# Kernel optimization log

Hardware: AMD Instinct MI355X
Metric: run time of the kernel (lower is better)

## Reference

```python
import jax, jax.numpy as jnp
import numpy as np

EPS = 1e-6

def _layernorm(x, g, b):
    mu = jnp.mean(x, axis=-1, keepdims=True)
    var = jnp.mean(jnp.square(x - mu), axis=-1, keepdims=True)
    return (x - mu) * jax.lax.rsqrt(var + EPS) * g + b

def _mhsa(xq, xk, xv, mask, Wq, bq, Wk, bk, Wv, bv, Wo, bo, num_heads):
    B, Nq, D = xq.shape
    Nk = xk.shape[1]
    dh = D // num_heads
    # project then split heads: [B, N, D] -> [B, H, N, dh]
    def split(x, W, b, N):
        return (x @ W + b).reshape(B, N, num_heads, dh).transpose(0, 2, 1, 3)
    q = split(xq, Wq, bq, Nq)
    k = split(xk, Wk, bk, Nk)
    v = split(xv, Wv, bv, Nk)
    scores = jnp.einsum('bhnd,bhmd->bhnm', q, k) / jnp.sqrt(jnp.float32(dh))
    if mask is not None:
        scores = scores + mask * (-1e9)
    w = jax.nn.softmax(scores, axis=-1)
    out = jnp.einsum('bhnm,bhmd->bhnd', w, v)          # [B,H,Nq,dh]
    out = out.transpose(0, 2, 1, 3).reshape(B, Nq, D)  # concat heads
    return out @ Wo + bo

def setup_inputs() -> dict:
    B, N, D, FF = 2, 2048, 512, 2048
    key = jax.random.key(0)
    ks = jax.random.split(key, 32)
    std = 0.02
    p = {}
    p['inputs'] = jax.random.normal(ks[0], (B, N, D), jnp.float32)
    p['enc_output'] = jax.random.normal(ks[1], (B, N, D), jnp.float32)
    # causal look-ahead mask: 1 where masked (future positions)
    p['look_ahead_mask'] = jnp.triu(jnp.ones((N, N), jnp.float32), k=1)[None, None]
    p['padding_mask'] = jnp.zeros((B, 1, 1, N), jnp.float32)
    i = 2
    for pre in ('q1', 'k1', 'v1', 'o1', 'q2', 'k2', 'v2', 'o2'):
        p[pre + '_w'] = jax.random.normal(ks[i], (D, D), jnp.float32) * std; i += 1
        p[pre + '_b'] = jnp.zeros((D,), jnp.float32)
    p['f1_w'] = jax.random.normal(ks[i], (D, FF), jnp.float32) * std; i += 1
    p['f1_b'] = jnp.zeros((FF,), jnp.float32)
    p['f2_w'] = jax.random.normal(ks[i], (FF, D), jnp.float32) * std; i += 1
    p['f2_b'] = jnp.zeros((D,), jnp.float32)
    for ln in ('ln1', 'ln2', 'ln3'):
        p[ln + '_g'] = jnp.ones((D,), jnp.float32)
        p[ln + '_b'] = jnp.zeros((D,), jnp.float32)
    p['training'] = 0
    return p

def reference(inputs, enc_output, look_ahead_mask, padding_mask,
              q1_w, q1_b, k1_w, k1_b, v1_w, v1_b, o1_w, o1_b,
              q2_w, q2_b, k2_w, k2_b, v2_w, v2_b, o2_w, o2_b,
              f1_w, f1_b, f2_w, f2_b,
              ln1_g, ln1_b, ln2_g, ln2_b, ln3_g, ln3_b,
              training):
    H = 8
    # self-attention (q=k=v=inputs), causal mask; dropout inactive (eval)
    attn1 = _mhsa(inputs, inputs, inputs, look_ahead_mask,
                  q1_w, q1_b, k1_w, k1_b, v1_w, v1_b, o1_w, o1_b, H)
    out1 = _layernorm(inputs + attn1, ln1_g, ln1_b)
    # cross attention: NOTE original arg order -> q=enc, k=enc, v=out1
    attn2 = _mhsa(enc_output, enc_output, out1, padding_mask,
                  q2_w, q2_b, k2_w, k2_b, v2_w, v2_b, o2_w, o2_b, H)
    out2 = _layernorm(out1 + attn2, ln2_g, ln2_b)
    ffn = jax.nn.relu(out2 @ f1_w + f1_b) @ f2_w + f2_b
    return _layernorm(out2 + ffn, ln3_g, ln3_b)
```

## Files before the change

kernel.cpp:

```cpp
#include <hip/hip_runtime.h>

typedef __attribute__((ext_vector_type(8))) _Float16 half8;
typedef __attribute__((ext_vector_type(4))) _Float16 half4;
typedef __attribute__((ext_vector_type(2))) _Float16 half2_t;
typedef __attribute__((ext_vector_type(2))) __fp16 fp16x2;
typedef __attribute__((ext_vector_type(4))) float f32x4;

#define AS1 __attribute__((address_space(1)))
#define AS3 __attribute__((address_space(3)))

constexpr int SEQ = 2048, DM = 512, FFD = 2048, NH = 8, DH = 64;
constexpr int M = 2 * SEQ;
constexpr float QSCALE = 0.125f * 1.4426950408889634f;

__global__ __launch_bounds__(256)
void preproc(const float* __restrict__ q1_w, const float* __restrict__ k1_w,
             const float* __restrict__ v1_w, const float* __restrict__ o1_w,
             const float* __restrict__ q2_w, const float* __restrict__ k2_w,
             const float* __restrict__ v2_w, const float* __restrict__ o2_w,
             const float* __restrict__ f1_w, const float* __restrict__ f2_w,
             _Float16* __restrict__ qk1t, _Float16* __restrict__ v1t,
             _Float16* __restrict__ o1t, _Float16* __restrict__ qk2t,
             _Float16* __restrict__ v2t, _Float16* __restrict__ o2t,
             _Float16* __restrict__ f1t, _Float16* __restrict__ f2t,
             const float* __restrict__ q1_b, const float* __restrict__ k1_b,
             const float* __restrict__ q2_b, const float* __restrict__ k2_b,
             float* __restrict__ qk1b, float* __restrict__ qk2b,
             const float* __restrict__ inp, const float* __restrict__ enc,
             _Float16* __restrict__ xh, _Float16* __restrict__ eh) {
    __shared__ _Float16 tile[64 * 65];
    const int j = blockIdx.x, tid = threadIdx.x;
    if (j < 1024) {
        const float* src; _Float16* dst; int K, N, n0, k0;
        if (j < 512) {
            int w8 = j >> 6, t = j & 63;
            K = 512; N = 512; n0 = (t & 7) * 64; k0 = (t >> 3) * 64;
            switch (w8) {
                case 0: src = q1_w; dst = qk1t; break;
                case 1: src = k1_w; dst = qk1t + 512 * 512; break;
                case 2: src = v1_w; dst = v1t; break;
                case 3: src = o1_w; dst = o1t; break;
                case 4: src = q2_w; dst = qk2t; break;
                case 5: src = k2_w; dst = qk2t + 512 * 512; break;
                case 6: src = v2_w; dst = v2t; break;
                default: src = o2_w; dst = o2t; break;
            }
        } else if (j < 768) {
            int t = j - 512; K = 512; N = 2048;
            n0 = (t % 32) * 64; k0 = (t / 32) * 64; src = f1_w; dst = f1t;
        } else {
            int t = j - 768; K = 2048; N = 512;
            n0 = (t % 8) * 64; k0 = (t / 8) * 64; src = f2_w; dst = f2t;
        }
        int c = tid & 63, r4 = tid >> 6;
        for (int i = 0; i < 16; i++) {
            int r = r4 * 16 + i;
            tile[r * 65 + c] = (_Float16)src[(size_t)(k0 + r) * N + n0 + c];
        }
        __syncthreads();
        for (int i = 0; i < 16; i++) {
            int r = r4 * 16 + i;
            dst[(size_t)(n0 + r) * K + k0 + c] = tile[c * 65 + r];
        }
    } else if (j == 1024) {
        for (int i = tid; i < 512; i += 256) { qk1b[i] = q1_b[i]; qk1b[512 + i] = k1_b[i]; }
    } else if (j == 1025) {
        for (int i = tid; i < 512; i += 256) { qk2b[i] = q2_b[i]; qk2b[512 + i] = k2_b[i]; }
    } else {
        int k = j - 1026;
        const float* s = (k < 1024) ? inp : enc;
        _Float16* d = (k < 1024) ? xh : eh;
        size_t base = (size_t)(k & 1023) * 2048 + tid * 8;
        f32x4 a = *(const f32x4*)(s + base);
        f32x4 b2 = *(const f32x4*)(s + base + 4);
        half8 h;
        h[0] = (_Float16)a[0]; h[1] = (_Float16)a[1];
        h[2] = (_Float16)a[2]; h[3] = (_Float16)a[3];
        h[4] = (_Float16)b2[0]; h[5] = (_Float16)b2[1];
        h[6] = (_Float16)b2[2]; h[7] = (_Float16)b2[3];
        *(half8*)(d + base) = h;
    }
}

template<int BM, int BN, int WM, int WN, bool RELU, int EPI, int SPLIT>
__global__ __launch_bounds__(256)
void gemm_tn(const _Float16* __restrict__ A, const _Float16* __restrict__ Bt,
             const float* __restrict__ bias,
             float* __restrict__ outF, _Float16* __restrict__ outH,
             _Float16* __restrict__ Qh, _Float16* __restrict__ Kh,
             const _Float16* __restrict__ A2, const _Float16* __restrict__ Bt2,
             const float* __restrict__ bias2,
             _Float16* __restrict__ Qh2, _Float16* __restrict__ Kh2,
             int Mtot, int N, int K) {
    constexpr int ROWS = BM + BN;
    __shared__ _Float16 smem[ROWS * 64];
    constexpr int AF = WM / 16, BF = WN / 16;
    constexpr int WROW = BM / WM;
    const int tid = threadIdx.x;
    const int wid = tid >> 6, lid = tid & 63;
    const int wr = (wid % WROW) * WM;
    const int wc = (wid / WROW) * WN;
    const int mi = lid & 15, qd = lid >> 4;
    const int gx = gridDim.x, gy = gridDim.y;
    const int L = blockIdx.y * gx + blockIdx.x;
    const int by = L % gy, bx = L / gy;
    const int m0 = by * BM, n0 = bx * BN;
    const int Kc = K / SPLIT;
    const int kbase = (SPLIT > 1) ? blockIdx.z * Kc : 0;
    const int job = (EPI == 4) ? blockIdx.z : 0;
    const _Float16* Ap = ((EPI == 4 && job) ? A2 : A) + (size_t)m0 * K + kbase;
    const _Float16* Bp = ((EPI == 4 && job) ? Bt2 : Bt) + (size_t)n0 * K + kbase;
    const float* bsel = (EPI == 4 && job) ? bias2 : bias;
    const int lrow = lid >> 3;
    const int gblk = (lid & 7) ^ ((lid >> 3) & 7);
    auto stage = [&](int kt) {
        #pragma unroll
        for (int l = 0; l < BM / 32; l++) {
            int c = l * 4 + wid;
            int row = c * 8 + lrow;
            __builtin_amdgcn_global_load_lds(
                (const AS1 unsigned int*)(Ap + (size_t)row * K + kt * 64 + gblk * 8),
                (AS3 unsigned int*)&smem[c * 512], 16, 0, 0);
        }
        #pragma unroll
        for (int l = 0; l < BN / 32; l++) {
            int c = l * 4 + wid;
            int row = c * 8 + lrow;
            __builtin_amdgcn_global_load_lds(
                (const AS1 unsigned int*)(Bp + (size_t)row * K + kt * 64 + gblk * 8),
                (AS3 unsigned int*)&smem[BM * 64 + c * 512], 16, 0, 0);
        }
    };
    f32x4 acc[AF][BF] = {};
    const int NIT = Kc / 64;
    stage(0);
    __builtin_amdgcn_s_waitcnt(0x0F70);
    __syncthreads();
    for (int t = 0; t < NIT; t++) {
        #pragma unroll
        for (int h = 0; h < 2; h++) {
            const int sA = ((4 * h + qd) ^ (mi & 7)) * 8;
            half8 af[AF], bfr[BF];
            #pragma unroll
            for (int i = 0; i < AF; i++)
                af[i] = *(const half8*)&smem[(wr + i * 16 + mi) * 64 + sA];
            #pragma unroll
            for (int j = 0; j < BF; j++)
                bfr[j] = *(const half8*)&smem[(BM + wc + j * 16 + mi) * 64 + sA];
            #pragma unroll
            for (int i = 0; i < AF; i++)
                #pragma unroll
                for (int j = 0; j < BF; j++)
                    acc[i][j] = __builtin_amdgcn_mfma_f32_16x16x32_f16(af[i], bfr[j], acc[i][j], 0, 0, 0);
        }
        if (t + 1 < NIT) {
            __syncthreads();
            stage(t + 1);
            __builtin_amdgcn_s_waitcnt(0x0F70);
            __syncthreads();
        }
    }
    float* oF = outF;
    if (SPLIT > 1 && outF) oF = outF + (size_t)blockIdx.z * Mtot * N;
    _Float16* oH = outH;
    if (EPI == 5) oH = outH + (size_t)blockIdx.z * Mtot * N;
    const bool doBias = bsel && (SPLIT == 1 || blockIdx.z == 0);
    #pragma unroll
    for (int i = 0; i < AF; i++) {
        #pragma unroll
        for (int j = 0; j < BF; j++) {
            #pragma unroll
            for (int r = 0; r < 4; r++) {
                int row = m0 + wr + i * 16 + qd * 4 + r;
                int col = n0 + wc + j * 16 + mi;
                float v = acc[i][j][r];
                if (EPI == 3) {
                    v += bsel[row];
                    outH[(size_t)row * N + col] = (_Float16)v;
                } else if (EPI == 4) {
                    if (doBias) v += bsel[col];
                    int hh = (col >> 6) & 7, d = col & 63;
                    int bb = row >> 11, n = row & 2047;
                    size_t idx = (((size_t)bb * 8 + hh) * SEQ + n) * 64 + d;
                    if (col < 512) (job ? Qh2 : Qh)[idx] = (_Float16)(v * QSCALE);
                    else           (job ? Kh2 : Kh)[idx] = (_Float16)v;
                } else if (EPI == 5) {
                    if (doBias) v += bsel[col];
                    oH[(size_t)row * N + col] = (_Float16)v;
                } else {
                    if (doBias) v += bsel[col];
                    if (RELU) v = fmaxf(v, 0.f);
                    size_t off = (size_t)row * N + col;
                    if (oF) oF[off] = v;
                    if (outH) outH[off] = (_Float16)v;
                }
            }
        }
    }
}

template<bool CAUSAL>
__global__ __launch_bounds__(256)
void attn_chunk(const _Float16* __restrict__ Qh, const _Float16* __restrict__ Kh,
                const _Float16* __restrict__ VT, int ldv,
                _Float16* __restrict__ Opart, float* __restrict__ Lpart) {
    const int qt = blockIdx.x, bh = blockIdx.y, c = blockIdx.z;
    int t0, stp, n;
    if (CAUSAL) {
        if (c > qt) return;
        t0 = c; stp = 4; n = (qt - c) / 4 + 1;
    } else {
        t0 = c * 8; stp = 1; n = 8;
    }
    __shared__ _Float16 QPs[64 * 64];
    __shared__ _Float16 Ks[2][64 * 64];
    __shared__ _Float16 Vs[2][64 * 64];
    const int tid = threadIdx.x, w = tid >> 6, lane = tid & 63;
    const int mi = lane & 15, qd = lane >> 4;
    const int qbase = qt * 64;
    const int b = bh >> 3, h = bh & 7;
    const _Float16* Qp = Qh + ((size_t)bh * SEQ + qbase) * 64;
    const _Float16* Kp = Kh + (size_t)bh * SEQ * 64;
    const _Float16* Vp = VT + (size_t)(h * 64) * ldv + (size_t)b * SEQ;
    const int r0 = tid >> 3, blk = tid & 7;
    const int sw = (blk ^ (r0 & 7)) * 8;
    const int lrow = lane >> 3;
    const int gblk = (lane & 7) ^ ((lane >> 3) & 7);
    const int f0 = (qd ^ (mi & 7)) * 8;
    const int f1 = ((qd + 4) ^ (mi & 7)) * 8;

    {
        half8 q0 = *(const half8*)(Qp + r0 * 64 + blk * 8);
        half8 q1 = *(const half8*)(Qp + (r0 + 32) * 64 + blk * 8);
        *(half8*)&QPs[r0 * 64 + sw] = q0;
        *(half8*)&QPs[(r0 + 32) * 64 + sw] = q1;
    }
    auto stageKV = [&](int t, int buf) {
        #pragma unroll
        for (int l = 0; l < 2; l++) {
            int cc = l * 4 + w;
            int row = cc * 8 + lrow;
            __builtin_amdgcn_global_load_lds(
                (const AS1 unsigned int*)(Kp + ((size_t)(t * 64 + row)) * 64 + gblk * 8),
                (AS3 unsigned int*)&Ks[buf][cc * 512], 16, 0, 0);
            __builtin_amdgcn_global_load_lds(
                (const AS1 unsigned int*)(Vp + (size_t)row * ldv + t * 64 + gblk * 8),
                (AS3 unsigned int*)&Vs[buf][cc * 512], 16, 0, 0);
        }
    };
    stageKV(t0, 0);
    __builtin_amdgcn_s_waitcnt(0x0F70);
    __syncthreads();
    half8 qb0 = *(half8*)&QPs[(w * 16 + mi) * 64 + f0];
    half8 qb1 = *(half8*)&QPs[(w * 16 + mi) * 64 + f1];
    f32x4 oacc[4] = {};
    float lacc = 0.f;
    for (int i = 0; i < n; i++) {
        const int t = t0 + i * stp;
        if (i + 1 < n) stageKV(t0 + (i + 1) * stp, (i + 1) & 1);
        const _Float16* ksb = Ks[i & 1];
        const _Float16* vsb = Vs[i & 1];
        f32x4 s[4];
        #pragma unroll
        for (int j = 0; j < 4; j++) {
            half8 ka0 = *(const half8*)&ksb[(j * 16 + mi) * 64 + f0];
            half8 ka1 = *(const half8*)&ksb[(j * 16 + mi) * 64 + f1];
            f32x4 a = {};
            a = __builtin_amdgcn_mfma_f32_16x16x32_f16(ka0, qb0, a, 0, 0, 0);
            a = __builtin_amdgcn_mfma_f32_16x16x32_f16(ka1, qb1, a, 0, 0, 0);
            s[j] = a;
        }
        if (CAUSAL && t == qt) {
            int qg = qbase + w * 16 + mi;
            #pragma unroll
            for (int j = 0; j < 4; j++)
                #pragma unroll
                for (int r = 0; r < 4; r++) {
                    int key = t * 64 + j * 16 + qd * 4 + r;
                    if (key > qg) s[j][r] = -1e30f;
                }
        }
        #pragma unroll
        for (int j = 0; j < 4; j++)
            #pragma unroll
            for (int r = 0; r < 4; r++) {
                float pv = __builtin_amdgcn_exp2f(s[j][r]);
                s[j][r] = pv;
                lacc += pv;
            }
        #pragma unroll
        for (int j = 0; j < 4; j++) {
            fp16x2 lo = __builtin_amdgcn_cvt_pkrtz(s[j][0], s[j][1]);
            fp16x2 hi = __builtin_amdgcn_cvt_pkrtz(s[j][2], s[j][3]);
            half2_t lo2 = __builtin_bit_cast(half2_t, lo);
            half2_t hi2 = __builtin_bit_cast(half2_t, hi);
            half4 pq;
            pq[0] = lo2[0]; pq[1] = lo2[1]; pq[2] = hi2[0]; pq[3] = hi2[1];
            int blkp = (2 * j + (qd >> 1)) ^ (mi & 7);
            *(half4*)&QPs[(w * 16 + mi) * 64 + blkp * 8 + (qd & 1) * 4] = pq;
        }
        half8 pa0 = *(half8*)&QPs[(w * 16 + mi) * 64 + f0];
        half8 pa1 = *(half8*)&QPs[(w * 16 + mi) * 64 + f1];
        #pragma unroll
        for (int j = 0; j < 4; j++) {
            half8 vb0 = *(const half8*)&vsb[(j * 16 + mi) * 64 + f0];
            half8 vb1 = *(const half8*)&vsb[(j * 16 + mi) * 64 + f1];
            oacc[j] = __builtin_amdgcn_mfma_f32_16x16x32_f16(pa0, vb0, oacc[j], 0, 0, 0);
            oacc[j] = __builtin_amdgcn_mfma_f32_16x16x32_f16(pa1, vb1, oacc[j], 0, 0, 0);
        }
        __builtin_amdgcn_s_waitcnt(0x0F70);
        __syncthreads();
    }
    const size_t tb = (((size_t)c * 16 + bh) * 32 + qt) * 4096;
    #pragma unroll
    for (int j = 0; j < 4; j++)
        #pragma unroll
        for (int r = 0; r < 4; r++)
            Opart[tb + (size_t)(w * 16 + qd * 4 + r) * 64 + j * 16 + mi] = (_Float16)oacc[j][r];
    lacc += __shfl_xor(lacc, 16, 64);
    lacc += __shfl_xor(lacc, 32, 64);
    if (qd == 0)
        Lpart[(((size_t)c * 16 + bh) * 32 + qt) * 64 + w * 16 + mi] = lacc;
}

template<bool CAUSAL>
__global__ __launch_bounds__(256)
void attn_combine(const _Float16* __restrict__ Opart, const float* __restrict__ Lpart,
                  _Float16* __restrict__ O) {
    const int qt = blockIdx.x, bh = blockIdx.y;
    const int b = bh >> 3, h = bh & 7;
    const int NC = CAUSAL ? min(qt + 1, 4) : 4;
    const int d = threadIdx.x & 63;
    const int rr = threadIdx.x >> 6;
    for (int it = 0; it < 16; it++) {
        int q = it * 4 + rr;
        float lsum = 0.f, acc = 0.f;
        for (int cc = 0; cc < NC; cc++) {
            lsum += Lpart[(((size_t)cc * 16 + bh) * 32 + qt) * 64 + q];
            acc += (float)Opart[(((size_t)cc * 16 + bh) * 32 + qt) * 4096 + (size_t)q * 64 + d];
        }
        int qrow = qt * 64 + q;
        O[((size_t)(b * SEQ + qrow)) * 512 + h * 64 + d] = (_Float16)(acc / lsum);
    }
}

template<typename RT>
__global__ __launch_bounds__(256)
void add_ln(const RT* __restrict__ res, const _Float16* __restrict__ y,
            size_t pstride, int nparts,
            const float* __restrict__ g, const float* __restrict__ bb,
            float* __restrict__ outF, _Float16* __restrict__ outH) {
    int row = blockIdx.x;
    int tid = threadIdx.x;
    size_t base = (size_t)row * 512;
    float x0 = (float)res[base + tid];
    float x1 = (float)res[base + tid + 256];
    for (int s = 0; s < nparts; s++) {
        x0 += (float)y[s * pstride + base + tid];
        x1 += (float)y[s * pstride + base + tid + 256];
    }
    float s = x0 + x1, sq = x0 * x0 + x1 * x1;
    #pragma unroll
    for (int off = 32; off > 0; off >>= 1) {
        s += __shfl_xor(s, off, 64);
        sq += __shfl_xor(sq, off, 64);
    }
    __shared__ float ls[4], lq[4];
    int w = tid >> 6;
    if ((tid & 63) == 0) { ls[w] = s; lq[w] = sq; }
    __syncthreads();
    s = ls[0] + ls[1] + ls[2] + ls[3];
    sq = lq[0] + lq[1] + lq[2] + lq[3];
    float mu = s * (1.f / 512.f);
    float var = sq * (1.f / 512.f) - mu * mu;
    float rs = rsqrtf(var + 1e-6f);
    float o0 = (x0 - mu) * rs * g[tid] + bb[tid];
    float o1 = (x1 - mu) * rs * g[tid + 256] + bb[tid + 256];
    if (outF) { outF[base + tid] = o0; outF[base + tid + 256] = o1; }
    if (outH) { outH[base + tid] = (_Float16)o0; outH[base + tid + 256] = (_Float16)o1; }
}

extern "C" void kernel_launch(void* const* d_in, const int* in_sizes, int n_in,
                              void* d_out, int out_size, void* d_ws, size_t ws_size,
                              hipStream_t stream) {
    (void)in_sizes; (void)n_in; (void)out_size; (void)ws_size;
    const float* inp  = (const float*)d_in[0];
    const float* enc  = (const float*)d_in[1];
    const float* q1_w = (const float*)d_in[4];
    const float* q1_b = (const float*)d_in[5];
    const float* k1_w = (const float*)d_in[6];
    const float* k1_b = (const float*)d_in[7];
    const float* v1_w = (const float*)d_in[8];
    const float* v1_b = (const float*)d_in[9];
    const float* o1_w = (const float*)d_in[10];
    const float* o1_b = (const float*)d_in[11];
    const float* q2_w = (const float*)d_in[12];
    const float* q2_b = (const float*)d_in[13];
    const float* k2_w = (const float*)d_in[14];
    const float* k2_b = (const float*)d_in[15];
    const float* v2_w = (const float*)d_in[16];
    const float* v2_b = (const float*)d_in[17];
    const float* o2_w = (const float*)d_in[18];
    const float* o2_b = (const float*)d_in[19];
    const float* f1_w = (const float*)d_in[20];
    const float* f1_b = (const float*)d_in[21];
    const float* f2_w = (const float*)d_in[22];
    const float* f2_b = (const float*)d_in[23];
    const float* ln1_g = (const float*)d_in[24];
    const float* ln1_b = (const float*)d_in[25];
    const float* ln2_g = (const float*)d_in[26];
    const float* ln2_b = (const float*)d_in[27];
    const float* ln3_g = (const float*)d_in[28];
    const float* ln3_b = (const float*)d_in[29];

    char* p = (char*)d_ws;
    auto alloc = [&](size_t bytes) { char* r = p; p += (bytes + 255) & ~(size_t)255; return (void*)r; };
    _Float16* xh    = (_Float16*)alloc((size_t)M * DM * 2);
    _Float16* eh    = (_Float16*)alloc((size_t)M * DM * 2);
    _Float16* qk1t  = (_Float16*)alloc((size_t)1024 * DM * 2);
    _Float16* v1t   = (_Float16*)alloc((size_t)DM * DM * 2);
    _Float16* o1t   = (_Float16*)alloc((size_t)DM * DM * 2);
    _Float16* qk2t  = (_Float16*)alloc((size_t)1024 * DM * 2);
    _Float16* v2t   = (_Float16*)alloc((size_t)DM * DM * 2);
    _Float16* o2t   = (_Float16*)alloc((size_t)DM * DM * 2);
    _Float16* f1t   = (_Float16*)alloc((size_t)FFD * DM * 2);
    _Float16* f2t   = (_Float16*)alloc((size_t)DM * FFD * 2);
    float* qk1b     = (float*)alloc(1024 * 4);
    float* qk2b     = (float*)alloc(1024 * 4);
    _Float16* Qh1   = (_Float16*)alloc((size_t)M * DM * 2);
    _Float16* Kh1   = (_Float16*)alloc((size_t)M * DM * 2);
    _Float16* Qh2   = (_Float16*)alloc((size_t)M * DM * 2);
    _Float16* Kh2   = (_Float16*)alloc((size_t)M * DM * 2);
    _Float16* V1T   = (_Float16*)alloc((size_t)DM * M * 2);
    _Float16* V2T   = (_Float16*)alloc((size_t)DM * M * 2);
    _Float16* Ah    = (_Float16*)alloc((size_t)M * DM * 2);
    _Float16* Ph    = (_Float16*)alloc((size_t)2 * M * DM * 2);
    float* Lbuf     = (float*)alloc((size_t)4 * 16 * 32 * 64 * 4);
    _Float16* out1h = (_Float16*)alloc((size_t)M * DM * 2);
    _Float16* out2h = (_Float16*)alloc((size_t)M * DM * 2);
    _Float16* hh    = (_Float16*)alloc((size_t)M * FFD * 2);
    _Float16* OpH   = (_Float16*)alloc((size_t)4 * 16 * 32 * 4096 * 2);
    const size_t PS = (size_t)M * DM;

    dim3 t256(256);
    preproc<<<dim3(1026 + 2048), t256, 0, stream>>>(
        q1_w, k1_w, v1_w, o1_w, q2_w, k2_w, v2_w, o2_w, f1_w, f2_w,
        qk1t, v1t, o1t, qk2t, v2t, o2t, f1t, f2t,
        q1_b, k1_b, q2_b, k2_b, qk1b, qk2b, inp, enc, xh, eh);

    gemm_tn<128, 64, 64, 32, false, 4, 1><<<dim3(16, 32, 2), t256, 0, stream>>>(
        xh, qk1t, qk1b, nullptr, nullptr, Qh1, Kh1,
        eh, qk2t, qk2b, Qh2, Kh2, M, 1024, 512);
    gemm_tn<64, 64, 32, 32, false, 3, 1><<<dim3(64, 8), t256, 0, stream>>>(
        v1t, xh, v1_b, nullptr, V1T, nullptr, nullptr,
        nullptr, nullptr, nullptr, nullptr, nullptr, 512, M, 512);

    attn_chunk<true><<<dim3(32, 16, 4), t256, 0, stream>>>(Qh1, Kh1, V1T, M, OpH, Lbuf);
    attn_combine<true><<<dim3(32, 16), t256, 0, stream>>>(OpH, Lbuf, Ah);
    gemm_tn<64, 64, 32, 32, false, 5, 2><<<dim3(8, 64, 2), t256, 0, stream>>>(
        Ah, o1t, o1_b, nullptr, Ph, nullptr, nullptr,
        nullptr, nullptr, nullptr, nullptr, nullptr, M, 512, 512);
    add_ln<float><<<dim3(M), t256, 0, stream>>>(inp, Ph, PS, 2, ln1_g, ln1_b, nullptr, out1h);

    gemm_tn<64, 64, 32, 32, false, 3, 1><<<dim3(64, 8), t256, 0, stream>>>(
        v2t, out1h, v2_b, nullptr, V2T, nullptr, nullptr,
        nullptr, nullptr, nullptr, nullptr, nullptr, 512, M, 512);
    attn_chunk<false><<<dim3(32, 16, 4), t256, 0, stream>>>(Qh2, Kh2, V2T, M, OpH, Lbuf);
    attn_combine<false><<<dim3(32, 16), t256, 0, stream>>>(OpH, Lbuf, Ah);
    gemm_tn<64, 64, 32, 32, false, 5, 2><<<dim3(8, 64, 2), t256, 0, stream>>>(
        Ah, o2t, o2_b, nullptr, Ph, nullptr, nullptr,
        nullptr, nullptr, nullptr, nullptr, nullptr, M, 512, 512);
    add_ln<_Float16><<<dim3(M), t256, 0, stream>>>(out1h, Ph, PS, 2, ln2_g, ln2_b, nullptr, out2h);

    gemm_tn<128, 64, 64, 32, true, 0, 1><<<dim3(32, 32), t256, 0, stream>>>(
        out2h, f1t, f1_b, nullptr, hh, nullptr, nullptr,
        nullptr, nullptr, nullptr, nullptr, nullptr, M, 2048, 512);
    gemm_tn<64, 64, 32, 32, false, 5, 2><<<dim3(8, 64, 2), t256, 0, stream>>>(
        hh, f2t, f2_b, nullptr, Ph, nullptr, nullptr,
        nullptr, nullptr, nullptr, nullptr, nullptr, M, 512, 2048);
    add_ln<_Float16><<<dim3(M), t256, 0, stream>>>(out2h, Ph, PS, 2, ln3_g, ln3_b, (float*)d_out, nullptr);
}
```

Baseline: 332.3 us.

## Replace split-KV attention and combine pass with single monolithic attention kernel

Merges the chunked attention kernel and its combine kernel into one kernel in which each block iterates over all key tiles and normalizes its output directly. For the causal pass, query tiles are interleaved so long and short tiles pair up for load balance. This removes the partial-output and partial-sum round trip through global memory and one launch per attention. In exchange the grid shrinks by a factor of four, which reduces parallelism and lengthens each block's serial loop.

```diff
diff --git a/kernel.cpp b/kernel.cpp
--- a/kernel.cpp
+++ b/kernel.cpp
@@ -201,20 +201,16 @@
 
 template<bool CAUSAL>
 __global__ __launch_bounds__(256)
-void attn_chunk(const _Float16* __restrict__ Qh, const _Float16* __restrict__ Kh,
-                const _Float16* __restrict__ VT, int ldv,
-                _Float16* __restrict__ Opart, float* __restrict__ Lpart) {
-    const int qt = blockIdx.x, bh = blockIdx.y, c = blockIdx.z;
-    int t0, stp, n;
-    if (CAUSAL) {
-        if (c > qt) return;
-        t0 = c; stp = 4; n = (qt - c) / 4 + 1;
-    } else {
-        t0 = c * 8; stp = 1; n = 8;
-    }
+void attn_mono(const _Float16* __restrict__ Qh, const _Float16* __restrict__ Kh,
+               const _Float16* __restrict__ VT, int ldv,
+               _Float16* __restrict__ O) {
+    const int x = blockIdx.x, bh = blockIdx.y;
+    const int qt = CAUSAL ? ((x & 1) ? (x >> 1) : (31 - (x >> 1))) : x;
+    const int nt = CAUSAL ? (qt + 1) : 32;
     __shared__ _Float16 QPs[64 * 64];
     __shared__ _Float16 Ks[2][64 * 64];
     __shared__ _Float16 Vs[2][64 * 64];
+    __shared__ float Lsh[64];
     const int tid = threadIdx.x, w = tid >> 6, lane = tid & 63;
     const int mi = lane & 15, qd = lane >> 4;
     const int qbase = qt * 64;
@@ -248,18 +244,17 @@
                 (AS3 unsigned int*)&Vs[buf][cc * 512], 16, 0, 0);
         }
     };
-    stageKV(t0, 0);
+    stageKV(0, 0);
     __builtin_amdgcn_s_waitcnt(0x0F70);
     __syncthreads();
     half8 qb0 = *(half8*)&QPs[(w * 16 + mi) * 64 + f0];
     half8 qb1 = *(half8*)&QPs[(w * 16 + mi) * 64 + f1];
     f32x4 oacc[4] = {};
     float lacc = 0.f;
-    for (int i = 0; i < n; i++) {
-        const int t = t0 + i * stp;
-        if (i + 1 < n) stageKV(t0 + (i + 1) * stp, (i + 1) & 1);
-        const _Float16* ksb = Ks[i & 1];
-        const _Float16* vsb = Vs[i & 1];
+    for (int t = 0; t < nt; t++) {
+        if (t + 1 < nt) stageKV(t + 1, (t + 1) & 1);
+        const _Float16* ksb = Ks[t & 1];
+        const _Float16* vsb = Vs[t & 1];
         f32x4 s[4];
         #pragma unroll
         for (int j = 0; j < 4; j++) {
@@ -311,36 +306,18 @@
         __builtin_amdgcn_s_waitcnt(0x0F70);
         __syncthreads();
     }
-    const size_t tb = (((size_t)c * 16 + bh) * 32 + qt) * 4096;
-    #pragma unroll
-    for (int j = 0; j < 4; j++)
-        #pragma unroll
-        for (int r = 0; r < 4; r++)
-            Opart[tb + (size_t)(w * 16 + qd * 4 + r) * 64 + j * 16 + mi] = (_Float16)oacc[j][r];
     lacc += __shfl_xor(lacc, 16, 64);
     lacc += __shfl_xor(lacc, 32, 64);
-    if (qd == 0)
-        Lpart[(((size_t)c * 16 + bh) * 32 + qt) * 64 + w * 16 + mi] = lacc;
-}
-
-template<bool CAUSAL>
-__global__ __launch_bounds__(256)
-void attn_combine(const _Float16* __restrict__ Opart, const float* __restrict__ Lpart,
-                  _Float16* __restrict__ O) {
-    const int qt = blockIdx.x, bh = blockIdx.y;
-    const int b = bh >> 3, h = bh & 7;
-    const int NC = CAUSAL ? min(qt + 1, 4) : 4;
-    const int d = threadIdx.x & 63;
-    const int rr = threadIdx.x >> 6;
-    for (int it = 0; it < 16; it++) {
-        int q = it * 4 + rr;
-        float lsum = 0.f, acc = 0.f;
-        for (int cc = 0; cc < NC; cc++) {
-            lsum += Lpart[(((size_t)cc * 16 + bh) * 32 + qt) * 64 + q];
-            acc += (float)Opart[(((size_t)cc * 16 + bh) * 32 + qt) * 4096 + (size_t)q * 64 + d];
-        }
-        int qrow = qt * 64 + q;
-        O[((size_t)(b * SEQ + qrow)) * 512 + h * 64 + d] = (_Float16)(acc / lsum);
+    if (qd == 0) Lsh[w * 16 + mi] = lacc;
+    __syncthreads();
+    #pragma unroll
+    for (int r = 0; r < 4; r++) {
+        float rl = 1.f / Lsh[w * 16 + qd * 4 + r];
+        int qrow = qbase + w * 16 + qd * 4 + r;
+        size_t obase = ((size_t)(b * SEQ + qrow)) * 512 + h * 64;
+        #pragma unroll
+        for (int j = 0; j < 4; j++)
+            O[obase + j * 16 + mi] = (_Float16)(oacc[j][r] * rl);
     }
 }
 
@@ -435,11 +412,9 @@
     _Float16* V2T   = (_Float16*)alloc((size_t)DM * M * 2);
     _Float16* Ah    = (_Float16*)alloc((size_t)M * DM * 2);
     _Float16* Ph    = (_Float16*)alloc((size_t)2 * M * DM * 2);
-    float* Lbuf     = (float*)alloc((size_t)4 * 16 * 32 * 64 * 4);
     _Float16* out1h = (_Float16*)alloc((size_t)M * DM * 2);
     _Float16* out2h = (_Float16*)alloc((size_t)M * DM * 2);
     _Float16* hh    = (_Float16*)alloc((size_t)M * FFD * 2);
-    _Float16* OpH   = (_Float16*)alloc((size_t)4 * 16 * 32 * 4096 * 2);
     const size_t PS = (size_t)M * DM;
 
     dim3 t256(256);
@@ -455,8 +430,7 @@
         v1t, xh, v1_b, nullptr, V1T, nullptr, nullptr,
         nullptr, nullptr, nullptr, nullptr, nullptr, 512, M, 512);
 
-    attn_chunk<true><<<dim3(32, 16, 4), t256, 0, stream>>>(Qh1, Kh1, V1T, M, OpH, Lbuf);
-    attn_combine<true><<<dim3(32, 16), t256, 0, stream>>>(OpH, Lbuf, Ah);
+    attn_mono<true><<<dim3(32, 16), t256, 0, stream>>>(Qh1, Kh1, V1T, M, Ah);
     gemm_tn<64, 64, 32, 32, false, 5, 2><<<dim3(8, 64, 2), t256, 0, stream>>>(
         Ah, o1t, o1_b, nullptr, Ph, nullptr, nullptr,
         nullptr, nullptr, nullptr, nullptr, nullptr, M, 512, 512);
@@ -465,8 +439,7 @@
     gemm_tn<64, 64, 32, 32, false, 3, 1><<<dim3(64, 8), t256, 0, stream>>>(
         v2t, out1h, v2_b, nullptr, V2T, nullptr, nullptr,
         nullptr, nullptr, nullptr, nullptr, nullptr, 512, M, 512);
-    attn_chunk<false><<<dim3(32, 16, 4), t256, 0, stream>>>(Qh2, Kh2, V2T, M, OpH, Lbuf);
-    attn_combine<false><<<dim3(32, 16), t256, 0, stream>>>(OpH, Lbuf, Ah);
+    attn_mono<false><<<dim3(32, 16), t256, 0, stream>>>(Qh2, Kh2, V2T, M, Ah);
     gemm_tn<64, 64, 32, 32, false, 5, 2><<<dim3(8, 64, 2), t256, 0, stream>>>(
         Ah, o2t, o2_b, nullptr, Ph, nullptr, nullptr,
         nullptr, nullptr, nullptr, nullptr, nullptr, M, 512, 512);
```

After: 322.2 us. 3.0% less time.
